# Optimization experiments

Hardware: AMD Instinct MI355X
Metric: run time of the kernel (lower is better)

The kernel has to match this reference:

```python
import jax, jax.numpy as jnp
import numpy as np
from jax import lax

T, B, H, NF, FS = 512, 128, 512, 128, 5  # max_seq_len, batch, hidden, num_filters, filter_size


def setup_inputs() -> dict:
    key = jax.random.key(0)
    ks = jax.random.split(key, 16)
    inp = {
        "encoder_output": jax.random.normal(ks[0], (T, B, H), dtype=jnp.float32),
        "lengths": jax.random.randint(ks[1], (B,), 1, T + 1, dtype=jnp.int64 if jax.config.jax_enable_x64 else jnp.int32),
    }
    for w in range(1, FS + 1):
        inp[f"conv_w{w}"] = jax.random.normal(ks[1 + w], (NF, 1, H, w), dtype=jnp.float32) * 0.02
        inp[f"conv_b{w}"] = jnp.zeros((NF,), dtype=jnp.float32)
    inp["fc1_w"] = jax.random.normal(ks[12], (100, FS * NF), dtype=jnp.float32) * 0.05
    inp["fc1_b"] = jnp.zeros((100,), dtype=jnp.float32)
    inp["fc2_w"] = jax.random.normal(ks[13], (1, 100), dtype=jnp.float32) * 0.1
    inp["fc2_b"] = jnp.zeros((1,), dtype=jnp.float32)
    return inp


def _raw_reshape(x, L):
    # Faithful to torch .contiguous().view(1,1,H,-1) on a [L,H] slice:
    # row-major flatten of first L rows, reshaped to [H, L], zero-padded to [H, T].
    flat = x.reshape(-1)                       # [T*H]
    h = jnp.arange(H)[:, None]                 # [H,1]
    l = jnp.arange(T)[None, :]                 # [1,T]
    return jnp.where(l < L, flat[h * L + l], 0.0)  # [H,T]


def reference(encoder_output, lengths,
              conv_w1, conv_b1, conv_w2, conv_b2, conv_w3, conv_b3,
              conv_w4, conv_b4, conv_w5, conv_b5,
              fc1_w, fc1_b, fc2_w, fc2_b):
    # encoder_output: [T, B, H]; per-sample raw reshape to [H, T] (length-dependent)
    X = jax.vmap(_raw_reshape, in_axes=(1, 0))(encoder_output, lengths)  # [B,H,T]
    X4 = X[:, None, :, :]                                               # [B,1,H,T]
    Leff = jnp.maximum(lengths, FS)  # torch code zero-pads width to >= filter_size
    conv_ws = [conv_w1, conv_w2, conv_w3, conv_w4, conv_w5]
    conv_bs = [conv_b1, conv_b2, conv_b3, conv_b4, conv_b5]
    pools = []
    for w in range(1, FS + 1):
        out = lax.conv_general_dilated(
            X4, conv_ws[w - 1], window_strides=(1, 1), padding='VALID',
            dimension_numbers=('NCHW', 'OIHW', 'NCHW'))          # [B,NF,1,T-w+1]
        r = jax.nn.relu(out[:, :, 0, :] + conv_bs[w - 1][None, :, None])  # [B,NF,Tw]
        tpos = jnp.arange(T - w + 1)
        valid = tpos[None, :] < (Leff - w + 1)[:, None]          # [B,Tw]
        r = jnp.where(valid[:, None, :], r, 0.0)                 # relu>=0, so 0 is safe for max
        pools.append(r.max(axis=2))                              # [B,NF]
    feat = jnp.concatenate(pools, axis=1)                        # [B,FS*NF]
    fc1 = feat @ fc1_w.T + fc1_b
    fc2 = fc1 @ fc2_w.T + fc2_b
    probs = jax.nn.sigmoid(fc2)                                  # [B,1]
    return probs[:, None, :]                                     # [B,1,1] == torch.stack of [1,1]
```

## Files before the change

### kernel.cpp

```cpp
#include <hip/hip_runtime.h>
#include <hip/hip_bf16.h>

#define TT 512
#define BB 128
#define HH 512
#define NFC 128

typedef short v8s __attribute__((ext_vector_type(8)));
typedef float v4f __attribute__((ext_vector_type(4)));

__device__ __forceinline__ unsigned short f2bf(float x) {
    unsigned u = __float_as_uint(x);
    unsigned r = (u + 0x7fffu + ((u >> 16) & 1u)) >> 16;
    return (unsigned short)r;
}

__global__ void prep_all(const float* __restrict__ enc, const int* __restrict__ lengths,
                         unsigned short* __restrict__ Xg,
                         const float* __restrict__ w1, const float* __restrict__ w2,
                         const float* __restrict__ w3, const float* __restrict__ w4,
                         const float* __restrict__ w5, unsigned short* __restrict__ Wg,
                         float* __restrict__ pools,
                         const float* __restrict__ fc1w, const float* __restrict__ fc1b,
                         const float* __restrict__ fc2w, const float* __restrict__ fc2b,
                         float* __restrict__ v, int* __restrict__ wl) {
    int blk = blockIdx.x;
    int tid = threadIdx.x;
    if (blk < 8192) {
        __shared__ float tile[64 * 65];
        int b = blk >> 6;
        int lc = (blk >> 3) & 7;
        int hc = blk & 7;
        int L = lengths[b];
        int Leff = L > 5 ? L : 5;
        int l0 = lc * 64, h0 = hc * 64;
        if (l0 >= Leff + 127) return;
        int lx = tid & 63;
        int hq = tid >> 6;
        #pragma unroll
        for (int r = 0; r < 16; ++r) {
            int hl = hq * 16 + r;
            int l = l0 + lx;
            float val = 0.f;
            if (l < L) {
                int i = (h0 + hl) * L + l;
                val = enc[(i >> 9) * (BB * HH) + b * HH + (i & 511)];
            }
            tile[hl * 65 + lx] = val;
        }
        __syncthreads();
        int hg = tid & 15;
        #pragma unroll
        for (int r = 0; r < 4; ++r) {
            int lloc = (tid >> 4) + r * 16;
            int n = b * 512 + l0 + lloc;
            ushort4 pk;
            pk.x = f2bf(tile[(hg * 4 + 0) * 65 + lloc]);
            pk.y = f2bf(tile[(hg * 4 + 1) * 65 + lloc]);
            pk.z = f2bf(tile[(hg * 4 + 2) * 65 + lloc]);
            pk.w = f2bf(tile[(hg * 4 + 3) * 65 + lloc]);
            *(ushort4*)&Xg[n * 512 + h0 + hg * 4] = pk;
        }
    } else if (blk < 12288) {
        int o = (blk - 8192) * 256 + tid;
        int j   = o & 7;
        int ln  = (o >> 3) & 63;
        int mi  = (o >> 9) & 3;
        int kt  = (o >> 11) & 15;
        int wmm = (o >> 15) & 1;
        int mtt = o >> 16;
        int row = mtt * 128 + wmm * 64 + mi * 16 + (ln & 15);
        int k   = kt * 32 + (ln >> 4) * 8 + j;
        int f = row >> 4, sl = row & 15;
        float val = 0.f;
        if (sl < 15) {
            int w, jj;
            if (sl < 1)       { w = 1; jj = sl; }
            else if (sl < 3)  { w = 2; jj = sl - 1; }
            else if (sl < 6)  { w = 3; jj = sl - 3; }
            else if (sl < 10) { w = 4; jj = sl - 6; }
            else              { w = 5; jj = sl - 10; }
            const float* wp = (w == 1) ? w1 : (w == 2) ? w2 : (w == 3) ? w3 : (w == 4) ? w4 : w5;
            val = wp[f * (HH * w) + k * w + jj];
        }
        Wg[o] = f2bf(val);
    } else if (blk < 12608) {
        int i = (blk - 12288) * 256 + tid;
        if (i < BB * 5 * NFC) pools[i] = 0.f;
    } else if (blk == 12608) {
        for (int k = tid; k < 640; k += 256) {
            float s = 0.f;
            for (int o = 0; o < 100; ++o) s += fc2w[o] * fc1w[o * 640 + k];
            v[k] = s;
        }
        if (tid == 0) {
            float c = fc2b[0];
            for (int o = 0; o < 100; ++o) c += fc2w[o] * fc1b[o];
            v[640] = c;
        }
    } else {
        __shared__ int cnt;
        if (tid == 0) cnt = 0;
        __syncthreads();
        for (int it = tid; it < 640; it += 256) {
            int b = it / 5, tt = it % 5;
            int L = lengths[b];
            int Leff = L > 5 ? L : 5;
            int n0 = tt * 124 - ((tt >> 2) * 112);
            if (n0 < Leff) {
                int pos = atomicAdd(&cnt, 1);
                wl[pos] = (b << 3) | tt;
            }
        }
        __syncthreads();
        if (tid == 0) wl[640] = cnt;
    }
}

#define STAGE_B(KT) do {                                                          \
    int bb_ = (((KT) + 2) & 3) * 4096;                                            \
    __builtin_amdgcn_global_load_lds(                                             \
        (const __attribute__((address_space(1))) unsigned int*)(gB + ((KT) + 2) * 32),            \
        (__attribute__((address_space(3))) unsigned int*)&ldsB[bb_ + sdst],       \
        16, 0, 0);                                                                \
    __builtin_amdgcn_global_load_lds(                                             \
        (const __attribute__((address_space(1))) unsigned int*)(gB + 16 * 512 + ((KT) + 2) * 32), \
        (__attribute__((address_space(3))) unsigned int*)&ldsB[bb_ + sdst + 512], \
        16, 0, 0);                                                                \
} while (0)

#define KT_BODY(KT, AC0, AC1, AC2, AC3, AL0, AL1, AL2, AL3, STAGE, LOADA, VMSTR) do { \
    if (STAGE) STAGE_B(KT);                                                       \
    asm volatile("s_waitcnt vmcnt(8)" ::: "memory");                              \
    __builtin_amdgcn_s_barrier();                                                 \
    int boff_ = ((KT) & 3) * 4096;                                                \
    v8s Bf0 = *(const v8s*)&ldsB[boff_ + (wn * 64 +  0 + llo) * 32 + psw * 8];    \
    v8s Bf1 = *(const v8s*)&ldsB[boff_ + (wn * 64 + 16 + llo) * 32 + psw * 8];    \
    v8s Bf2 = *(const v8s*)&ldsB[boff_ + (wn * 64 + 32 + llo) * 32 + psw * 8];    \
    v8s Bf3 = *(const v8s*)&ldsB[boff_ + (wn * 64 + 48 + llo) * 32 + psw * 8];    \
    asm volatile("s_waitcnt " VMSTR ::: "memory");                                \
    __builtin_amdgcn_sched_barrier(0);                                            \
    if (LOADA) {                                                                  \
        asm volatile("global_load_dwordx4 %0, %1, off"             : "=v"(AL0) : "v"(pAc) : "memory"); \
        asm volatile("global_load_dwordx4 %0, %1, off offset:1024" : "=v"(AL1) : "v"(pAc) : "memory"); \
        asm volatile("global_load_dwordx4 %0, %1, off offset:2048" : "=v"(AL2) : "v"(pAc) : "memory"); \
        asm volatile("global_load_dwordx4 %0, %1, off offset:3072" : "=v"(AL3) : "v"(pAc) : "memory"); \
        pAc += 2048;                                                              \
    }                                                                             \
    __builtin_amdgcn_s_setprio(1);                                                \
    acc[0][0] = __builtin_amdgcn_mfma_f32_16x16x32_bf16(AC0, Bf0, acc[0][0], 0, 0, 0); \
    acc[0][1] = __builtin_amdgcn_mfma_f32_16x16x32_bf16(AC0, Bf1, acc[0][1], 0, 0, 0); \
    acc[0][2] = __builtin_amdgcn_mfma_f32_16x16x32_bf16(AC0, Bf2, acc[0][2], 0, 0, 0); \
    acc[0][3] = __builtin_amdgcn_mfma_f32_16x16x32_bf16(AC0, Bf3, acc[0][3], 0, 0, 0); \
    acc[1][0] = __builtin_amdgcn_mfma_f32_16x16x32_bf16(AC1, Bf0, acc[1][0], 0, 0, 0); \
    acc[1][1] = __builtin_amdgcn_mfma_f32_16x16x32_bf16(AC1, Bf1, acc[1][1], 0, 0, 0); \
    acc[1][2] = __builtin_amdgcn_mfma_f32_16x16x32_bf16(AC1, Bf2, acc[1][2], 0, 0, 0); \
    acc[1][3] = __builtin_amdgcn_mfma_f32_16x16x32_bf16(AC1, Bf3, acc[1][3], 0, 0, 0); \
    acc[2][0] = __builtin_amdgcn_mfma_f32_16x16x32_bf16(AC2, Bf0, acc[2][0], 0, 0, 0); \
    acc[2][1] = __builtin_amdgcn_mfma_f32_16x16x32_bf16(AC2, Bf1, acc[2][1], 0, 0, 0); \
    acc[2][2] = __builtin_amdgcn_mfma_f32_16x16x32_bf16(AC2, Bf2, acc[2][2], 0, 0, 0); \
    acc[2][3] = __builtin_amdgcn_mfma_f32_16x16x32_bf16(AC2, Bf3, acc[2][3], 0, 0, 0); \
    acc[3][0] = __builtin_amdgcn_mfma_f32_16x16x32_bf16(AC3, Bf0, acc[3][0], 0, 0, 0); \
    acc[3][1] = __builtin_amdgcn_mfma_f32_16x16x32_bf16(AC3, Bf1, acc[3][1], 0, 0, 0); \
    acc[3][2] = __builtin_amdgcn_mfma_f32_16x16x32_bf16(AC3, Bf2, acc[3][2], 0, 0, 0); \
    acc[3][3] = __builtin_amdgcn_mfma_f32_16x16x32_bf16(AC3, Bf3, acc[3][3], 0, 0, 0); \
    __builtin_amdgcn_s_setprio(0);                                                \
} while (0)

__global__ __launch_bounds__(256, 4)
void conv_gemm(const unsigned short* __restrict__ Wg, const unsigned short* __restrict__ Xg,
               const int* __restrict__ lengths, const int* __restrict__ wl,
               const float* __restrict__ cb1, const float* __restrict__ cb2,
               const float* __restrict__ cb3, const float* __restrict__ cb4,
               const float* __restrict__ cb5,
               float* __restrict__ pools) {
    __shared__ __align__(16) char smem[33024];
    unsigned short* ldsB = (unsigned short*)smem;
    float* Gs = (float*)smem;

    int cnt = wl[640];
    int g = blockIdx.x;
    int xcd = g & 7;
    int q = g >> 3;
    int mt = q & 15;
    int wk = (q >> 4) * 8 + xcd;
    if (wk >= cnt) return;
    int item = wl[wk];
    int b = item >> 3, tt = item & 7;
    int n0 = tt * 124 - ((tt >> 2) * 112);
    int L = lengths[b];
    int Leff = L > 5 ? L : 5;

    int tid = threadIdx.x;
    int wid = tid >> 6, lane = tid & 63;
    int wm = wid >> 1, wn = wid & 1;
    int llo = lane & 15, quad = lane >> 4;
    int psw = quad ^ ((llo >> 1) & 3);

    int nb0 = b * 512 + n0;

    v4f acc[4][4];
    #pragma unroll
    for (int i = 0; i < 4; ++i)
        #pragma unroll
        for (int j = 0; j < 4; ++j) acc[i][j] = v4f{0.f, 0.f, 0.f, 0.f};

    int srow = lane >> 2;
    int gchunk = (lane & 3) ^ ((lane >> 3) & 3);
    const unsigned short* gB = Xg + (nb0 + wid * 32 + srow) * 512 + gchunk * 8;
    int sdst = (wid * 32) * 32;

    const unsigned short* pA = Wg + (mt * 2 + wm) * 32768 + lane * 8;

    #pragma unroll
    for (int p = 0; p < 2; ++p) {
        #pragma unroll
        for (int q2 = 0; q2 < 2; ++q2) {
            __builtin_amdgcn_global_load_lds(
                (const __attribute__((address_space(1))) unsigned int*)(gB + q2 * (16 * 512) + p * 32),
                (__attribute__((address_space(3))) unsigned int*)&ldsB[p * 4096 + sdst + q2 * 512],
                16, 0, 0);
        }
    }
    v8s AfA0, AfA1, AfA2, AfA3;
    v8s AfB0, AfB1, AfB2, AfB3;
    asm volatile("global_load_dwordx4 %0, %1, off"             : "=v"(AfA0) : "v"(pA) : "memory");
    asm volatile("global_load_dwordx4 %0, %1, off offset:1024" : "=v"(AfA1) : "v"(pA) : "memory");
    asm volatile("global_load_dwordx4 %0, %1, off offset:2048" : "=v"(AfA2) : "v"(pA) : "memory");
    asm volatile("global_load_dwordx4 %0, %1, off offset:3072" : "=v"(AfA3) : "v"(pA) : "memory");
    const unsigned short* pAc = pA + 2048;

    #pragma unroll 1
    for (int t = 0; t < 7; ++t) {
        int kte = 2 * t;
        KT_BODY(kte,     AfA0, AfA1, AfA2, AfA3, AfB0, AfB1, AfB2, AfB3, true, true, "vmcnt(2)");
        KT_BODY(kte + 1, AfB0, AfB1, AfB2, AfB3, AfA0, AfA1, AfA2, AfA3, true, true, "vmcnt(2)");
    }
    KT_BODY(14, AfA0, AfA1, AfA2, AfA3, AfB0, AfB1, AfB2, AfB3, false, true,  "vmcnt(0)");
    KT_BODY(15, AfB0, AfB1, AfB2, AfB3, AfA0, AfA1, AfA2, AfA3, false, false, "vmcnt(0)");

    __syncthreads();

    #pragma unroll
    for (int phase = 0; phase < 2; ++phase) {
        if (wm == phase) {
            #pragma unroll
            for (int mi = 0; mi < 4; ++mi)
                #pragma unroll
                for (int ni = 0; ni < 4; ++ni)
                    #pragma unroll
                    for (int r = 0; r < 4; ++r)
                        Gs[(mi * 16 + quad * 4 + r) * 129 + wn * 64 + ni * 16 + llo] = acc[mi][ni][r];
        }
        __syncthreads();
        {
            int fl = wid;
            int f = mt * 8 + phase * 4 + fl;
            float bias[5] = {cb1[f], cb2[f], cb3[f], cb4[f], cb5[f]};
            const int basew[5] = {0, 1, 3, 6, 10};
            const float* gbase = &Gs[(fl * 16) * 129 + lane];
            float vm[5];
            #pragma unroll
            for (int w = 1; w <= 5; ++w) {
                float s0 = 0.f, s1 = 0.f;
                #pragma unroll
                for (int j = 0; j < w; ++j) {
                    int o = basew[w - 1] * 129 + j * 130;
                    s0 += gbase[o];
                    s1 += gbase[o + 64];
                }
                int limv = Leff - w + 1 - n0;
                int lim = 128 - w; if (limv - 1 < lim) lim = limv - 1;
                float m = -1.f;
                if (lane <= lim)      m = fmaxf(m, fmaxf(s0 + bias[w - 1], 0.f));
                if (lane + 64 <= lim) m = fmaxf(m, fmaxf(s1 + bias[w - 1], 0.f));
                vm[w - 1] = m;
            }
            #pragma unroll
            for (int off = 32; off >= 1; off >>= 1) {
                #pragma unroll
                for (int w = 0; w < 5; ++w)
                    vm[w] = fmaxf(vm[w], __shfl_xor(vm[w], off));
            }
            if (lane == 0 && vm[0] >= 0.f) atomicMax((int*)&pools[(b * 5 + 0) * NFC + f], __float_as_int(vm[0]));
            if (lane == 1 && vm[1] >= 0.f) atomicMax((int*)&pools[(b * 5 + 1) * NFC + f], __float_as_int(vm[1]));
            if (lane == 2 && vm[2] >= 0.f) atomicMax((int*)&pools[(b * 5 + 2) * NFC + f], __float_as_int(vm[2]));
            if (lane == 3 && vm[3] >= 0.f) atomicMax((int*)&pools[(b * 5 + 3) * NFC + f], __float_as_int(vm[3]));
            if (lane == 4 && vm[4] >= 0.f) atomicMax((int*)&pools[(b * 5 + 4) * NFC + f], __float_as_int(vm[4]));
        }
        __syncthreads();
    }
}

__global__ void head(const float* __restrict__ pools, const float* __restrict__ v,
                     float* __restrict__ out) {
    int b = blockIdx.x;
    int tid = threadIdx.x;
    float s = 0.f;
    for (int k = tid; k < 640; k += 256) s += pools[b * 640 + k] * v[k];
    __shared__ float red[256];
    red[tid] = s;
    __syncthreads();
    for (int st = 128; st; st >>= 1) {
        if (tid < st) red[tid] += red[tid + st];
        __syncthreads();
    }
    if (tid == 0) out[b] = 1.f / (1.f + expf(-(red[0] + v[640])));
}

extern "C" void kernel_launch(void* const* d_in, const int* in_sizes, int n_in,
                              void* d_out, int out_size, void* d_ws, size_t ws_size,
                              hipStream_t stream) {
    const float* enc  = (const float*)d_in[0];
    const int* lens   = (const int*)d_in[1];
    const float* w1   = (const float*)d_in[2];
    const float* b1   = (const float*)d_in[3];
    const float* w2   = (const float*)d_in[4];
    const float* b2   = (const float*)d_in[5];
    const float* w3   = (const float*)d_in[6];
    const float* b3   = (const float*)d_in[7];
    const float* w4   = (const float*)d_in[8];
    const float* b4   = (const float*)d_in[9];
    const float* w5   = (const float*)d_in[10];
    const float* b5   = (const float*)d_in[11];
    const float* fc1w = (const float*)d_in[12];
    const float* fc1b = (const float*)d_in[13];
    const float* fc2w = (const float*)d_in[14];
    const float* fc2b = (const float*)d_in[15];
    float* out = (float*)d_out;

    unsigned short* Xg = (unsigned short*)d_ws;
    unsigned short* Wg = Xg + 33554432;
    float* pools  = (float*)(Wg + 1048576);
    float* vbuf   = pools + 81920;
    int* wlist    = (int*)(vbuf + 641);

    prep_all<<<12610, 256, 0, stream>>>(enc, lens, Xg, w1, w2, w3, w4, w5, Wg, pools,
                                        fc1w, fc1b, fc2w, fc2b, vbuf, wlist);
    conv_gemm<<<10240, 256, 0, stream>>>(Wg, Xg, lens, wlist, b1, b2, b3, b4, b5, pools);
    head<<<128, 256, 0, stream>>>(pools, vbuf, out);
}
```

Before: 343.2 us.

## Restructure conv GEMM main loop to two k-steps per barrier with deeper A prefetch

The main K loop now stages B tiles into LDS two k-steps at a time with one barrier per pair, instead of one barrier per k-step. The A fragments are prefetched two k-steps ahead into double register sets. A-fragment loads are issued after the MFMAs rather than before them. This halves the workgroup barriers and is meant to hide more global-load latency behind MFMA work. The hand-tuned vmcnt accounting becomes harder to get right, and a wrong count could read data before it has arrived.

```diff
diff --git a/kernel.cpp b/kernel.cpp
--- a/kernel.cpp
+++ b/kernel.cpp
@@ -117,55 +117,41 @@
     }
 }
 
-#define STAGE_B(KT) do {                                                          \
-    int bb_ = (((KT) + 2) & 3) * 4096;                                            \
-    __builtin_amdgcn_global_load_lds(                                             \
-        (const __attribute__((address_space(1))) unsigned int*)(gB + ((KT) + 2) * 32),            \
-        (__attribute__((address_space(3))) unsigned int*)&ldsB[bb_ + sdst],       \
-        16, 0, 0);                                                                \
-    __builtin_amdgcn_global_load_lds(                                             \
-        (const __attribute__((address_space(1))) unsigned int*)(gB + 16 * 512 + ((KT) + 2) * 32), \
-        (__attribute__((address_space(3))) unsigned int*)&ldsB[bb_ + sdst + 512], \
-        16, 0, 0);                                                                \
+#define GLDS(GP, LP) __builtin_amdgcn_global_load_lds(                            \
+    (const __attribute__((address_space(1))) unsigned int*)(GP),                  \
+    (__attribute__((address_space(3))) unsigned int*)(LP), 16, 0, 0)
+
+#define LOADA4(B0, B1, B2, B3, PTR) do {                                          \
+    asm volatile("global_load_dwordx4 %0, %1, off"             : "=v"(B0) : "v"(PTR) : "memory"); \
+    asm volatile("global_load_dwordx4 %0, %1, off offset:1024" : "=v"(B1) : "v"(PTR) : "memory"); \
+    asm volatile("global_load_dwordx4 %0, %1, off offset:2048" : "=v"(B2) : "v"(PTR) : "memory"); \
+    asm volatile("global_load_dwordx4 %0, %1, off offset:3072" : "=v"(B3) : "v"(PTR) : "memory"); \
 } while (0)
 
-#define KT_BODY(KT, AC0, AC1, AC2, AC3, AL0, AL1, AL2, AL3, STAGE, LOADA, VMSTR) do { \
-    if (STAGE) STAGE_B(KT);                                                       \
-    asm volatile("s_waitcnt vmcnt(8)" ::: "memory");                              \
-    __builtin_amdgcn_s_barrier();                                                 \
-    int boff_ = ((KT) & 3) * 4096;                                                \
-    v8s Bf0 = *(const v8s*)&ldsB[boff_ + (wn * 64 +  0 + llo) * 32 + psw * 8];    \
-    v8s Bf1 = *(const v8s*)&ldsB[boff_ + (wn * 64 + 16 + llo) * 32 + psw * 8];    \
-    v8s Bf2 = *(const v8s*)&ldsB[boff_ + (wn * 64 + 32 + llo) * 32 + psw * 8];    \
-    v8s Bf3 = *(const v8s*)&ldsB[boff_ + (wn * 64 + 48 + llo) * 32 + psw * 8];    \
-    asm volatile("s_waitcnt " VMSTR ::: "memory");                                \
-    __builtin_amdgcn_sched_barrier(0);                                            \
-    if (LOADA) {                                                                  \
-        asm volatile("global_load_dwordx4 %0, %1, off"             : "=v"(AL0) : "v"(pAc) : "memory"); \
-        asm volatile("global_load_dwordx4 %0, %1, off offset:1024" : "=v"(AL1) : "v"(pAc) : "memory"); \
-        asm volatile("global_load_dwordx4 %0, %1, off offset:2048" : "=v"(AL2) : "v"(pAc) : "memory"); \
-        asm volatile("global_load_dwordx4 %0, %1, off offset:3072" : "=v"(AL3) : "v"(pAc) : "memory"); \
-        pAc += 2048;                                                              \
-    }                                                                             \
-    __builtin_amdgcn_s_setprio(1);                                                \
-    acc[0][0] = __builtin_amdgcn_mfma_f32_16x16x32_bf16(AC0, Bf0, acc[0][0], 0, 0, 0); \
-    acc[0][1] = __builtin_amdgcn_mfma_f32_16x16x32_bf16(AC0, Bf1, acc[0][1], 0, 0, 0); \
-    acc[0][2] = __builtin_amdgcn_mfma_f32_16x16x32_bf16(AC0, Bf2, acc[0][2], 0, 0, 0); \
-    acc[0][3] = __builtin_amdgcn_mfma_f32_16x16x32_bf16(AC0, Bf3, acc[0][3], 0, 0, 0); \
-    acc[1][0] = __builtin_amdgcn_mfma_f32_16x16x32_bf16(AC1, Bf0, acc[1][0], 0, 0, 0); \
-    acc[1][1] = __builtin_amdgcn_mfma_f32_16x16x32_bf16(AC1, Bf1, acc[1][1], 0, 0, 0); \
-    acc[1][2] = __builtin_amdgcn_mfma_f32_16x16x32_bf16(AC1, Bf2, acc[1][2], 0, 0, 0); \
-    acc[1][3] = __builtin_amdgcn_mfma_f32_16x16x32_bf16(AC1, Bf3, acc[1][3], 0, 0, 0); \
-    acc[2][0] = __builtin_amdgcn_mfma_f32_16x16x32_bf16(AC2, Bf0, acc[2][0], 0, 0, 0); \
-    acc[2][1] = __builtin_amdgcn_mfma_f32_16x16x32_bf16(AC2, Bf1, acc[2][1], 0, 0, 0); \
-    acc[2][2] = __builtin_amdgcn_mfma_f32_16x16x32_bf16(AC2, Bf2, acc[2][2], 0, 0, 0); \
-    acc[2][3] = __builtin_amdgcn_mfma_f32_16x16x32_bf16(AC2, Bf3, acc[2][3], 0, 0, 0); \
-    acc[3][0] = __builtin_amdgcn_mfma_f32_16x16x32_bf16(AC3, Bf0, acc[3][0], 0, 0, 0); \
-    acc[3][1] = __builtin_amdgcn_mfma_f32_16x16x32_bf16(AC3, Bf1, acc[3][1], 0, 0, 0); \
-    acc[3][2] = __builtin_amdgcn_mfma_f32_16x16x32_bf16(AC3, Bf2, acc[3][2], 0, 0, 0); \
-    acc[3][3] = __builtin_amdgcn_mfma_f32_16x16x32_bf16(AC3, Bf3, acc[3][3], 0, 0, 0); \
-    __builtin_amdgcn_s_setprio(0);                                                \
+#define MFMA16(A0, A1, A2, A3) do {                                               \
+    acc[0][0] = __builtin_amdgcn_mfma_f32_16x16x32_bf16(A0, Bf0, acc[0][0], 0, 0, 0); \
+    acc[0][1] = __builtin_amdgcn_mfma_f32_16x16x32_bf16(A0, Bf1, acc[0][1], 0, 0, 0); \
+    acc[0][2] = __builtin_amdgcn_mfma_f32_16x16x32_bf16(A0, Bf2, acc[0][2], 0, 0, 0); \
+    acc[0][3] = __builtin_amdgcn_mfma_f32_16x16x32_bf16(A0, Bf3, acc[0][3], 0, 0, 0); \
+    acc[1][0] = __builtin_amdgcn_mfma_f32_16x16x32_bf16(A1, Bf0, acc[1][0], 0, 0, 0); \
+    acc[1][1] = __builtin_amdgcn_mfma_f32_16x16x32_bf16(A1, Bf1, acc[1][1], 0, 0, 0); \
+    acc[1][2] = __builtin_amdgcn_mfma_f32_16x16x32_bf16(A1, Bf2, acc[1][2], 0, 0, 0); \
+    acc[1][3] = __builtin_amdgcn_mfma_f32_16x16x32_bf16(A1, Bf3, acc[1][3], 0, 0, 0); \
+    acc[2][0] = __builtin_amdgcn_mfma_f32_16x16x32_bf16(A2, Bf0, acc[2][0], 0, 0, 0); \
+    acc[2][1] = __builtin_amdgcn_mfma_f32_16x16x32_bf16(A2, Bf1, acc[2][1], 0, 0, 0); \
+    acc[2][2] = __builtin_amdgcn_mfma_f32_16x16x32_bf16(A2, Bf2, acc[2][2], 0, 0, 0); \
+    acc[2][3] = __builtin_amdgcn_mfma_f32_16x16x32_bf16(A2, Bf3, acc[2][3], 0, 0, 0); \
+    acc[3][0] = __builtin_amdgcn_mfma_f32_16x16x32_bf16(A3, Bf0, acc[3][0], 0, 0, 0); \
+    acc[3][1] = __builtin_amdgcn_mfma_f32_16x16x32_bf16(A3, Bf1, acc[3][1], 0, 0, 0); \
+    acc[3][2] = __builtin_amdgcn_mfma_f32_16x16x32_bf16(A3, Bf2, acc[3][2], 0, 0, 0); \
+    acc[3][3] = __builtin_amdgcn_mfma_f32_16x16x32_bf16(A3, Bf3, acc[3][3], 0, 0, 0); \
 } while (0)
+
+#define BREAD(SLOT)                                                               \
+    v8s Bf0 = *(const v8s*)&ldsB[(SLOT) * 4096 + (wn * 64 +  0 + llo) * 32 + psw * 8]; \
+    v8s Bf1 = *(const v8s*)&ldsB[(SLOT) * 4096 + (wn * 64 + 16 + llo) * 32 + psw * 8]; \
+    v8s Bf2 = *(const v8s*)&ldsB[(SLOT) * 4096 + (wn * 64 + 32 + llo) * 32 + psw * 8]; \
+    v8s Bf3 = *(const v8s*)&ldsB[(SLOT) * 4096 + (wn * 64 + 48 + llo) * 32 + psw * 8];
 
 __global__ __launch_bounds__(256, 4)
 void conv_gemm(const unsigned short* __restrict__ Wg, const unsigned short* __restrict__ Xg,
@@ -212,32 +198,71 @@
 
     const unsigned short* pA = Wg + (mt * 2 + wm) * 32768 + lane * 8;
 
-    #pragma unroll
-    for (int p = 0; p < 2; ++p) {
-        #pragma unroll
-        for (int q2 = 0; q2 < 2; ++q2) {
-            __builtin_amdgcn_global_load_lds(
-                (const __attribute__((address_space(1))) unsigned int*)(gB + q2 * (16 * 512) + p * 32),
-                (__attribute__((address_space(3))) unsigned int*)&ldsB[p * 4096 + sdst + q2 * 512],
-                16, 0, 0);
-        }
-    }
+    GLDS(gB,                 &ldsB[0 * 4096 + sdst]);
+    GLDS(gB + 16 * 512,      &ldsB[0 * 4096 + sdst + 512]);
+    GLDS(gB + 32,            &ldsB[1 * 4096 + sdst]);
+    GLDS(gB + 16 * 512 + 32, &ldsB[1 * 4096 + sdst + 512]);
     v8s AfA0, AfA1, AfA2, AfA3;
     v8s AfB0, AfB1, AfB2, AfB3;
-    asm volatile("global_load_dwordx4 %0, %1, off"             : "=v"(AfA0) : "v"(pA) : "memory");
-    asm volatile("global_load_dwordx4 %0, %1, off offset:1024" : "=v"(AfA1) : "v"(pA) : "memory");
-    asm volatile("global_load_dwordx4 %0, %1, off offset:2048" : "=v"(AfA2) : "v"(pA) : "memory");
-    asm volatile("global_load_dwordx4 %0, %1, off offset:3072" : "=v"(AfA3) : "v"(pA) : "memory");
-    const unsigned short* pAc = pA + 2048;
+    LOADA4(AfA0, AfA1, AfA2, AfA3, pA);
+    {
+        const unsigned short* pA1 = pA + 2048;
+        LOADA4(AfB0, AfB1, AfB2, AfB3, pA1);
+    }
+    const unsigned short* pAc = pA + 4096;
 
     #pragma unroll 1
-    for (int t = 0; t < 7; ++t) {
-        int kte = 2 * t;
-        KT_BODY(kte,     AfA0, AfA1, AfA2, AfA3, AfB0, AfB1, AfB2, AfB3, true, true, "vmcnt(2)");
-        KT_BODY(kte + 1, AfB0, AfB1, AfB2, AfB3, AfA0, AfA1, AfA2, AfA3, true, true, "vmcnt(2)");
-    }
-    KT_BODY(14, AfA0, AfA1, AfA2, AfA3, AfB0, AfB1, AfB2, AfB3, false, true,  "vmcnt(0)");
-    KT_BODY(15, AfB0, AfB1, AfB2, AfB3, AfA0, AfA1, AfA2, AfA3, false, false, "vmcnt(0)");
+    for (int i = 0; i < 7; ++i) {
+        int sb = (i & 1) * 2;
+        int tb = 2 - sb;
+        asm volatile("s_waitcnt vmcnt(8)" ::: "memory");
+        __builtin_amdgcn_s_barrier();
+        {
+            const unsigned short* gs = gB + (2 * i + 2) * 32;
+            GLDS(gs,                 &ldsB[tb * 4096 + sdst]);
+            GLDS(gs + 16 * 512,      &ldsB[tb * 4096 + sdst + 512]);
+            GLDS(gs + 32,            &ldsB[(tb + 1) * 4096 + sdst]);
+            GLDS(gs + 16 * 512 + 32, &ldsB[(tb + 1) * 4096 + sdst + 512]);
+        }
+        {
+            BREAD(sb);
+            asm volatile("s_waitcnt vmcnt(8)" ::: "memory");
+            __builtin_amdgcn_sched_barrier(0);
+            __builtin_amdgcn_s_setprio(1);
+            MFMA16(AfA0, AfA1, AfA2, AfA3);
+            __builtin_amdgcn_s_setprio(0);
+            LOADA4(AfA0, AfA1, AfA2, AfA3, pAc);
+            pAc += 2048;
+        }
+        {
+            BREAD(sb + 1);
+            asm volatile("s_waitcnt vmcnt(8)" ::: "memory");
+            __builtin_amdgcn_sched_barrier(0);
+            __builtin_amdgcn_s_setprio(1);
+            MFMA16(AfB0, AfB1, AfB2, AfB3);
+            __builtin_amdgcn_s_setprio(0);
+            LOADA4(AfB0, AfB1, AfB2, AfB3, pAc);
+            pAc += 2048;
+        }
+    }
+    asm volatile("s_waitcnt vmcnt(8)" ::: "memory");
+    __builtin_amdgcn_s_barrier();
+    {
+        BREAD(2);
+        asm volatile("s_waitcnt vmcnt(4)" ::: "memory");
+        __builtin_amdgcn_sched_barrier(0);
+        __builtin_amdgcn_s_setprio(1);
+        MFMA16(AfA0, AfA1, AfA2, AfA3);
+        __builtin_amdgcn_s_setprio(0);
+    }
+    {
+        BREAD(3);
+        asm volatile("s_waitcnt vmcnt(0)" ::: "memory");
+        __builtin_amdgcn_sched_barrier(0);
+        __builtin_amdgcn_s_setprio(1);
+        MFMA16(AfB0, AfB1, AfB2, AfB3);
+        __builtin_amdgcn_s_setprio(0);
+    }
 
     __syncthreads();
 
```

Measured after the change: 344.3 us. About the same (+0.3%).
